# Performance work log

Measured on AMD Instinct MI355X. Metric: run time of the kernel, lower is better.

The kernel has to match this reference:

```python
import jax, jax.numpy as jnp
import numpy as np

VOCAB, EMB, HID, NCLS = 50000, 256, 512, 20
NCHARS, CEMB, CHID = 128, 64, 128
B, S, L = 128, 256, 16


def _gru(xw, h0, Wh, bh):
    """Run a GRU given precomputed input projections.
    xw: [N, T, 3H] = x @ Wi.T + bi (PyTorch gate order r,z,n)
    h0: [N, H]
    Returns (h_T [N,H], all_h [N,T,H])."""
    H = h0.shape[-1]
    def step(h, xw_t):
        gh = h @ Wh.T + bh  # [N, 3H]
        r = jax.nn.sigmoid(xw_t[:, :H] + gh[:, :H])
        z = jax.nn.sigmoid(xw_t[:, H:2 * H] + gh[:, H:2 * H])
        n = jnp.tanh(xw_t[:, 2 * H:] + r * gh[:, 2 * H:])
        h = (1.0 - z) * n + z * h
        return h, h
    hT, hs = jax.lax.scan(step, h0, jnp.swapaxes(xw, 0, 1))
    return hT, jnp.swapaxes(hs, 0, 1)


def setup_inputs() -> dict:
    key = jax.random.key(0)
    ks = jax.random.split(key, 16)
    sc = lambda *sh: 0.05
    inp = {}
    inp["x"] = jax.random.randint(ks[0], (B, S), 0, VOCAB)
    inp["x_chars"] = jax.random.randint(ks[1], (S, B, L), 0, NCHARS)
    inp["emb_w"] = jax.random.normal(ks[2], (VOCAB, EMB), jnp.float32) * 0.05
    inp["char_emb_w"] = jax.random.normal(ks[3], (NCHARS, CEMB), jnp.float32) * 0.05
    inp["char_Wi"] = jax.random.normal(ks[4], (3 * CHID, CEMB), jnp.float32) * 0.05
    inp["char_Wh"] = jax.random.normal(ks[5], (3 * CHID, CHID), jnp.float32) * 0.05
    inp["char_bi"] = jax.random.normal(ks[6], (3 * CHID,), jnp.float32) * 0.05
    inp["char_bh"] = jax.random.normal(ks[7], (3 * CHID,), jnp.float32) * 0.05
    D = EMB + CHID
    inp["gru_Wi"] = jax.random.normal(ks[8], (3 * HID, D), jnp.float32) * 0.05
    inp["gru_Wh"] = jax.random.normal(ks[9], (3 * HID, HID), jnp.float32) * 0.05
    inp["gru_bi"] = jax.random.normal(ks[10], (3 * HID,), jnp.float32) * 0.05
    inp["gru_bh"] = jax.random.normal(ks[11], (3 * HID,), jnp.float32) * 0.05
    inp["cls_W"] = jax.random.normal(ks[12], (NCLS, HID), jnp.float32) * 0.05
    inp["cls_b"] = jax.random.normal(ks[13], (NCLS,), jnp.float32) * 0.05
    return inp


def reference(x, x_chars, emb_w, char_emb_w, char_Wi, char_Wh, char_bi, char_bh,
              gru_Wi, gru_Wh, gru_bi, gru_bh, cls_W, cls_b):
    b, s = x.shape
    l = x_chars.shape[-1]
    # word embeddings [B,S,EMB]
    emb_x = emb_w[x]
    # char GRU: batch all S*B words at once (fuses the per-word Python loop)
    chid = char_Wh.shape[-1]
    flat = x_chars.reshape(s * b, l)           # [S*B, L]
    cemb = char_emb_w[flat]                    # [S*B, L, CEMB]
    cxw = jnp.einsum('ntd,gd->ntg', cemb, char_Wi) + char_bi
    h0c = jnp.zeros((s * b, chid), cemb.dtype)
    c_hT, _ = _gru(cxw, h0c, char_Wh, char_bh)  # [S*B, CHID]
    chars = jnp.swapaxes(c_hT.reshape(s, b, chid), 0, 1)  # [B,S,CHID]
    # word GRU over concat features
    feats = jnp.concatenate([emb_x, chars], axis=-1)       # [B,S,EMB+CHID]
    xw = jnp.einsum('btd,gd->btg', feats, gru_Wi) + gru_bi
    hid = gru_Wh.shape[-1]
    h0 = jnp.zeros((b, hid), feats.dtype)
    _, gru_out = _gru(xw, h0, gru_Wh, gru_bh)              # [B,S,HID]
    # dropout is identity in eval mode
    pred = jnp.einsum('bth,ch->btc', gru_out, cls_W) + cls_b
    return pred
```

## Files before the change

### kernel.cpp

```cpp
#include <hip/hip_runtime.h>
#include <cstdio>
#include <cstdint>

typedef __attribute__((ext_vector_type(8))) short short8;
typedef __attribute__((ext_vector_type(4))) float f32x4;

__device__ __forceinline__ f32x4 MFMA16(short8 a, short8 b, f32x4 c) {
  return __builtin_amdgcn_mfma_f32_16x16x32_bf16(a, b, c, 0, 0, 0);
}
__device__ __forceinline__ float bf2f(uint16_t u) {
  union { uint32_t u; float f; } v; v.u = ((uint32_t)u) << 16; return v.f;
}
__device__ __forceinline__ uint16_t f2bf(float f) {
  union { float f; uint32_t u; } v; v.f = f;
  uint32_t r = v.u + 0x7fffu + ((v.u >> 16) & 1u);
  return (uint16_t)(r >> 16);
}
__device__ __forceinline__ float fsig(float x) { return 1.0f / (1.0f + __expf(-x)); }
__device__ __forceinline__ float ftanh_(float x) { return 2.0f / (1.0f + __expf(-2.0f * x)) - 1.0f; }


#define OFF_CWI   0u
#define OFF_CWH   49152u
#define OFF_GWI   147456u
#define OFF_GWH   1327104u
#define OFF_CEMB  2899968u
#define OFF_CRZ   2916352u
#define OFF_CNI   2917376u
#define OFF_CNH   2917888u
#define OFF_WRZ   2918400u
#define OFF_WNI   2922496u
#define OFF_WNH   2924544u
#define OFF_CNT   2926592u
#define OFF_FEATS 3145728u
#define OFF_XW    28311552u
#define OFF_H     128974848u
#define WS_NEEDED 145752064ull

__global__ void k_prep(const float* __restrict__ cWi, const float* __restrict__ cWh,
                       const float* __restrict__ gWi, const float* __restrict__ gWh,
                       const float* __restrict__ cemb,
                       const float* __restrict__ cbi, const float* __restrict__ cbh,
                       const float* __restrict__ gbi, const float* __restrict__ gbh,
                       uint16_t* o_cWi, uint16_t* o_cWh, uint16_t* o_gWi, uint16_t* o_gWh,
                       uint16_t* o_cemb, float* o_crz, float* o_cni, float* o_cnh,
                       float* o_wrz, float* o_wni, float* o_wnh, unsigned* cnt)
{
  int g = blockIdx.x * 256 + threadIdx.x;
  int st = gridDim.x * 256;
  for (int i = g; i < 24576;  i += st) o_cWi[i] = f2bf(cWi[i]);
  for (int i = g; i < 49152;  i += st) o_cWh[i] = f2bf(cWh[i]);
  for (int i = g; i < 589824; i += st) o_gWi[i] = f2bf(gWi[i]);
  for (int i = g; i < 786432; i += st) o_gWh[i] = f2bf(gWh[i]);
  for (int i = g; i < 8192;   i += st) o_cemb[i] = f2bf(cemb[i]);
  for (int i = g; i < 256;  i += st) o_crz[i] = cbi[i] + cbh[i];
  for (int i = g; i < 128;  i += st) { o_cni[i] = cbi[256 + i]; o_cnh[i] = cbh[256 + i]; }
  for (int i = g; i < 1024; i += st) o_wrz[i] = gbi[i] + gbh[i];
  for (int i = g; i < 512;  i += st) { o_wni[i] = gbi[1024 + i]; o_wnh[i] = gbh[1024 + i]; }
  for (int i = g; i < 8192; i += st) cnt[i] = 0u;
}

__global__ void k_emb(const int* __restrict__ x, const float* __restrict__ embw,
                      uint16_t* __restrict__ feats)
{
  int n = blockIdx.x * 4 + (threadIdx.x >> 6);
  int lane = threadIdx.x & 63;
  int t = n >> 7, b = n & 127;
  int wid = x[b * 256 + t];
  float4 v = *(const float4*)(embw + (size_t)wid * 256 + lane * 4);
  uint16_t* dst = feats + (size_t)n * 384 + lane * 4;
  dst[0] = f2bf(v.x); dst[1] = f2bf(v.y); dst[2] = f2bf(v.z); dst[3] = f2bf(v.w);
}

__global__ __launch_bounds__(256, 1) void k_char(
    const int* __restrict__ xch, const uint16_t* __restrict__ cembw,
    const uint16_t* __restrict__ cWi, const uint16_t* __restrict__ cWh,
    const float* __restrict__ crz, const float* __restrict__ cni,
    const float* __restrict__ cnh, uint16_t* __restrict__ feats)
{
  extern __shared__ char lds[];
  uint16_t* WhL = (uint16_t*)lds;
  int*      idsL = (int*)(lds + 104448);
  uint16_t* hL  = (uint16_t*)(lds + 104448 + 4352);
  const int tid = threadIdx.x;
  const int wbase = blockIdx.x * 64;

  for (int i = tid; i < 384 * 16; i += 256) {
    int row = i >> 4, ch = i & 15;
    *(uint4*)(WhL + row * 136 + ch * 8) = *(const uint4*)(cWh + row * 128 + ch * 8);
  }
  for (int i = tid; i < 64 * 16; i += 256) {
    int w0 = i >> 4, p = i & 15;
    idsL[w0 * 17 + p] = xch[(wbase + w0) * 16 + p];
  }
  for (int i = tid; i < 64 * 136 / 2; i += 256) ((unsigned*)hL)[i] = 0u;
  __syncthreads();

  const int wv = tid >> 6, lane = tid & 63;
  const int q = lane >> 4, c = lane & 15;
  float br_[8], bz_[8], bni_[8], bnh_[8];
#pragma unroll
  for (int jb = 0; jb < 8; ++jb) {
    int j = jb * 16 + c;
    br_[jb] = crz[j]; bz_[jb] = crz[128 + j]; bni_[jb] = cni[j]; bnh_[jb] = cnh[j];
  }
  const int lwA = wv * 16 + c;
  const int lwD = wv * 16 + q * 4;

  for (int t = 0; t < 16; ++t) {
    f32x4 aRZ[16], aXN[8], aGN[8];
#pragma unroll
    for (int i = 0; i < 16; ++i) aRZ[i] = (f32x4)0.0f;
#pragma unroll
    for (int i = 0; i < 8; ++i) { aXN[i] = (f32x4)0.0f; aGN[i] = (f32x4)0.0f; }

    int id = idsL[lwA * 17 + t];
    const uint16_t* cerow = cembw + id * 64;
    short8 Ae0 = *(const short8*)(cerow + q * 8);
    short8 Ae1 = *(const short8*)(cerow + 32 + q * 8);
#pragma unroll
    for (int tl = 0; tl < 24; ++tl) {
      const uint16_t* wr = cWi + (tl * 16 + c) * 64 + q * 8;
      short8 B0 = *(const short8*)(wr);
      short8 B1 = *(const short8*)(wr + 32);
      if (tl < 16) { aRZ[tl] = MFMA16(Ae0, B0, aRZ[tl]); aRZ[tl] = MFMA16(Ae1, B1, aRZ[tl]); }
      else { aXN[tl - 16] = MFMA16(Ae0, B0, aXN[tl - 16]); aXN[tl - 16] = MFMA16(Ae1, B1, aXN[tl - 16]); }
    }
    short8 Ah[4];
#pragma unroll
    for (int kt = 0; kt < 4; ++kt) Ah[kt] = *(const short8*)(hL + lwA * 136 + kt * 32 + q * 8);
#pragma unroll
    for (int tl = 0; tl < 24; ++tl) {
#pragma unroll
      for (int kt = 0; kt < 4; ++kt) {
        short8 Bw = *(const short8*)(WhL + (tl * 16 + c) * 136 + kt * 32 + q * 8);
        if (tl < 16) aRZ[tl] = MFMA16(Ah[kt], Bw, aRZ[tl]);
        else aGN[tl - 16] = MFMA16(Ah[kt], Bw, aGN[tl - 16]);
      }
    }
#pragma unroll
    for (int jb = 0; jb < 8; ++jb) {
      int j = jb * 16 + c;
#pragma unroll
      for (int rg = 0; rg < 4; ++rg) {
        float r = fsig(aRZ[jb][rg] + br_[jb]);
        float z = fsig(aRZ[8 + jb][rg] + bz_[jb]);
        float n = ftanh_(aXN[jb][rg] + bni_[jb] + r * (aGN[jb][rg] + bnh_[jb]));
        int hoff = (lwD + rg) * 136 + j;
        float hold = bf2f(hL[hoff]);
        hL[hoff] = f2bf((1.0f - z) * n + z * hold);
      }
    }
  }
  __syncthreads();
  for (int i = tid; i < 64 * 128; i += 256) {
    int w0 = i >> 7, col = i & 127;
    feats[(size_t)(wbase + w0) * 384 + 256 + col] = hL[w0 * 136 + col];
  }
}

__global__ __launch_bounds__(256) void k_gemm_xw(
    const uint16_t* __restrict__ A, const uint16_t* __restrict__ Bm,
    uint16_t* __restrict__ C)
{
  __shared__ uint16_t AL[128 * 40];
  __shared__ uint16_t BL[128 * 40];
  const int tid = threadIdx.x;
  const int bm = blockIdx.x & 255, bn = blockIdx.x >> 8;
  const int m0 = bm * 128, n0 = bn * 128;
  const int wv = tid >> 6, lane = tid & 63, q = lane >> 4, c = lane & 15;
  const int vm = (wv >> 1) * 64, vn = (wv & 1) * 64;
  f32x4 acc[4][4];
#pragma unroll
  for (int mt = 0; mt < 4; ++mt)
#pragma unroll
    for (int nt = 0; nt < 4; ++nt) acc[mt][nt] = (f32x4)0.0f;

  for (int k0 = 0; k0 < 384; k0 += 32) {
    __syncthreads();
    for (int i2 = tid; i2 < 512; i2 += 256) {
      int row = i2 >> 2, cc = i2 & 3;
      *(uint4*)(AL + row * 40 + cc * 8) = *(const uint4*)(A + (size_t)(m0 + row) * 384 + k0 + cc * 8);
      *(uint4*)(BL + row * 40 + cc * 8) = *(const uint4*)(Bm + (size_t)(n0 + row) * 384 + k0 + cc * 8);
    }
    __syncthreads();
    short8 af[4], bfr[4];
#pragma unroll
    for (int mt = 0; mt < 4; ++mt) af[mt] = *(const short8*)(AL + (vm + mt * 16 + c) * 40 + q * 8);
#pragma unroll
    for (int nt = 0; nt < 4; ++nt) bfr[nt] = *(const short8*)(BL + (vn + nt * 16 + c) * 40 + q * 8);
#pragma unroll
    for (int mt = 0; mt < 4; ++mt)
#pragma unroll
      for (int nt = 0; nt < 4; ++nt) acc[mt][nt] = MFMA16(af[mt], bfr[nt], acc[mt][nt]);
  }
#pragma unroll
  for (int mt = 0; mt < 4; ++mt)
#pragma unroll
    for (int nt = 0; nt < 4; ++nt)
#pragma unroll
      for (int rg = 0; rg < 4; ++rg) {
        int m = m0 + vm + mt * 16 + q * 4 + rg;
        int n = n0 + vn + nt * 16 + c;
        C[(size_t)m * 1536 + n] = f2bf(acc[mt][nt][rg]);
      }
}

__global__ __launch_bounds__(64, 1) void k_gru(
    const uint16_t* __restrict__ xw, const uint16_t* __restrict__ gWh,
    const float* __restrict__ wrz, const float* __restrict__ wni,
    const float* __restrict__ wnh, uint16_t* __restrict__ H,
    unsigned* __restrict__ cnt)
{
  extern __shared__ char lds[];
  uint16_t* WhL = (uint16_t*)lds;
  const int tid = threadIdx.x;

  unsigned xcd;
  asm volatile("s_getreg_b32 %0, hwreg(HW_REG_XCC_ID, 0, 4)" : "=s"(xcd));
  unsigned* rdv = cnt + 4096;
  int myslot = 0;
  if (tid == 0) {
    myslot = (int)__hip_atomic_fetch_add(cnt + 4224 + xcd * 32, 1u, __ATOMIC_RELAXED, __HIP_MEMORY_SCOPE_AGENT);
    __hip_atomic_fetch_add(rdv, 1u, __ATOMIC_RELEASE, __HIP_MEMORY_SCOPE_AGENT);
  }
  myslot = __shfl(myslot, 0);
  {
    int sp = 0;
    while (__hip_atomic_load(rdv, __ATOMIC_ACQUIRE, __HIP_MEMORY_SCOPE_AGENT) < 128u) {
      __builtin_amdgcn_s_sleep(1);
      if (++sp > 10000000) break;
    }
  }
  unsigned G = 0, base = 0;
#pragma unroll
  for (int x2 = 0; x2 < 8; ++x2) {
    unsigned v = __hip_atomic_load(cnt + 4224 + x2 * 32, __ATOMIC_RELAXED, __HIP_MEMORY_SCOPE_AGENT) >> 4;
    if ((unsigned)x2 < xcd) base += v;
    G += v;
  }
  bool fastp; int gb, gc;
  if (G == 8u) { fastp = true; gb = (int)(base + ((unsigned)myslot >> 4)); gc = myslot & 15; }
  else         { fastp = false; gb = blockIdx.x & 7; gc = blockIdx.x >> 3; }

  const int m0 = gb * 16, j0 = gc * 32;
  unsigned* gflag  = cnt + ((gb * 16) << 5);
  unsigned* myflag = gflag + (gc << 5);
  unsigned* myCnt  = cnt + 4608 + (gb << 5);

  for (int i = tid; i < 96 * 64; i += 64) {
    int row = i >> 6, ch = i & 63;
    int gr = (row < 32) ? (j0 + row) : (row < 64) ? (512 + j0 + row - 32) : (1024 + j0 + row - 64);
    *(uint4*)(WhL + row * 520 + ch * 8) = *(const uint4*)(gWh + (size_t)gr * 512 + ch * 8);
  }
  const int q = tid >> 4, c = tid & 15;
  const int j1 = j0 + c, j2 = j0 + 16 + c;
  const float br0 = wrz[j1], br1 = wrz[j2];
  const float bz0 = wrz[512 + j1], bz1 = wrz[512 + j2];
  const float bi0 = wni[j1], bi1 = wni[j2];
  const float bh0 = wnh[j1], bh1 = wnh[j2];
  __syncthreads();

  uint16_t pf[4][6];
  {
    const uint16_t* xwt = xw + (size_t)m0 * 1536;
#pragma unroll
    for (int rg = 0; rg < 4; ++rg) {
      const uint16_t* rowp = xwt + (q * 4 + rg) * 1536;
      pf[rg][0] = rowp[j1];        pf[rg][1] = rowp[j2];
      pf[rg][2] = rowp[512 + j1];  pf[rg][3] = rowp[512 + j2];
      pf[rg][4] = rowp[1024 + j1]; pf[rg][5] = rowp[1024 + j2];
    }
  }
  float hold1[4] = {0.f, 0.f, 0.f, 0.f}, hold2[4] = {0.f, 0.f, 0.f, 0.f};

  for (int t = 0; t < 256; ++t) {
    f32x4 acc[6];
    float xn1[4], xn2[4];
#pragma unroll
    for (int rg = 0; rg < 4; ++rg) {
      acc[0][rg] = bf2f(pf[rg][0]); acc[1][rg] = bf2f(pf[rg][1]);
      acc[2][rg] = bf2f(pf[rg][2]); acc[3][rg] = bf2f(pf[rg][3]);
      acc[4][rg] = 0.0f; acc[5][rg] = 0.0f;
      xn1[rg] = bf2f(pf[rg][4]); xn2[rg] = bf2f(pf[rg][5]);
    }
    if (t > 0) {
      const uint16_t* hp = H + (size_t)((t - 1) * 128 + m0) * 512 + c * 512;
#pragma unroll 4
      for (int kt = 0; kt < 16; ++kt) {
        short8 a = *(const short8*)(hp + kt * 32 + q * 8);
#pragma unroll
        for (int tl = 0; tl < 6; ++tl) {
          short8 b = *(const short8*)(WhL + (tl * 16 + c) * 520 + kt * 32 + q * 8);
          acc[tl] = MFMA16(a, b, acc[tl]);
        }
      }
    }
    uint16_t* hcur = H + (size_t)(t * 128 + m0) * 512;
#pragma unroll
    for (int rg = 0; rg < 4; ++rg) {
      int m = q * 4 + rg;
      float r0 = fsig(acc[0][rg] + br0);
      float z0 = fsig(acc[2][rg] + bz0);
      float n0 = ftanh_(xn1[rg] + bi0 + r0 * (acc[4][rg] + bh0));
      float h0 = (1.0f - z0) * n0 + z0 * hold1[rg];
      hold1[rg] = h0;
      hcur[m * 512 + j1] = f2bf(h0);
      float r1 = fsig(acc[1][rg] + br1);
      float z1 = fsig(acc[3][rg] + bz1);
      float n1 = ftanh_(xn2[rg] + bi1 + r1 * (acc[5][rg] + bh1));
      float h1 = (1.0f - z1) * n1 + z1 * hold2[rg];
      hold2[rg] = h1;
      hcur[m * 512 + j2] = f2bf(h1);
    }
    if (t == 255) break;
    const unsigned tgt = (unsigned)(t + 1);
    if (fastp) {
      asm volatile("s_waitcnt vmcnt(0)" ::: "memory");
      if (tid == 0)
        __hip_atomic_store(myflag, tgt, __ATOMIC_RELAXED, __HIP_MEMORY_SCOPE_AGENT);
      {
        const uint16_t* xwn = xw + (size_t)((t + 1) * 128 + m0) * 1536;
#pragma unroll
        for (int rg = 0; rg < 4; ++rg) {
          const uint16_t* rowp = xwn + (q * 4 + rg) * 1536;
          pf[rg][0] = rowp[j1];        pf[rg][1] = rowp[j2];
          pf[rg][2] = rowp[512 + j1];  pf[rg][3] = rowp[512 + j2];
          pf[rg][4] = rowp[1024 + j1]; pf[rg][5] = rowp[1024 + j2];
        }
      }
      unsigned* watch = gflag + ((tid & 15) << 5);
      int sp = 0;
      for (;;) {
        unsigned v = __hip_atomic_load(watch, __ATOMIC_RELAXED, __HIP_MEMORY_SCOPE_AGENT);
        if (__all((int)(v >= tgt))) break;
        if (++sp > 2000000) break;
      }
      asm volatile("" ::: "memory");
    } else {
      {
        const uint16_t* xwn = xw + (size_t)((t + 1) * 128 + m0) * 1536;
#pragma unroll
        for (int rg = 0; rg < 4; ++rg) {
          const uint16_t* rowp = xwn + (q * 4 + rg) * 1536;
          pf[rg][0] = rowp[j1];        pf[rg][1] = rowp[j2];
          pf[rg][2] = rowp[512 + j1];  pf[rg][3] = rowp[512 + j2];
          pf[rg][4] = rowp[1024 + j1]; pf[rg][5] = rowp[1024 + j2];
        }
      }
      __threadfence();
      if (tid == 0) __hip_atomic_fetch_add(myCnt, 1u, __ATOMIC_RELAXED, __HIP_MEMORY_SCOPE_AGENT);
      const unsigned target = tgt * 16u;
      int sp = 0;
      while (__hip_atomic_load(myCnt, __ATOMIC_RELAXED, __HIP_MEMORY_SCOPE_AGENT) < target) {
        __builtin_amdgcn_s_sleep(1);
        if (++sp > 2000000) break;
      }
      __threadfence();
    }
  }
}

__global__ void k_cls(const uint16_t* __restrict__ H, const float* __restrict__ W,
                      const float* __restrict__ bb, float* __restrict__ out)
{
  int g = blockIdx.x * 256 + threadIdx.x;
  int c = g % 20, row = g / 20;
  int t = row >> 7, b = row & 127;
  const uint16_t* hp = H + (size_t)row * 512;
  const float* wp = W + c * 512;
  float acc = 0.0f;
  for (int i = 0; i < 512; i += 8) {
    uint4 hv = *(const uint4*)(hp + i);
    float4 w0 = *(const float4*)(wp + i);
    float4 w1 = *(const float4*)(wp + i + 4);
    acc += bf2f((uint16_t)hv.x) * w0.x + bf2f((uint16_t)(hv.x >> 16)) * w0.y
         + bf2f((uint16_t)hv.y) * w0.z + bf2f((uint16_t)(hv.y >> 16)) * w0.w
         + bf2f((uint16_t)hv.z) * w1.x + bf2f((uint16_t)(hv.z >> 16)) * w1.y
         + bf2f((uint16_t)hv.w) * w1.z + bf2f((uint16_t)(hv.w >> 16)) * w1.w;
  }
  out[((size_t)b * 256 + t) * 20 + c] = acc + bb[c];
}

extern "C" void kernel_launch(void* const* d_in, const int* in_sizes, int n_in,
                              void* d_out, int out_size, void* d_ws, size_t ws_size,
                              hipStream_t stream) {
  (void)in_sizes; (void)n_in; (void)out_size;
  const int*   x     = (const int*)d_in[0];
  const int*   xch   = (const int*)d_in[1];
  const float* embw  = (const float*)d_in[2];
  const float* cembw = (const float*)d_in[3];
  const float* cWi   = (const float*)d_in[4];
  const float* cWh   = (const float*)d_in[5];
  const float* cbi   = (const float*)d_in[6];
  const float* cbh   = (const float*)d_in[7];
  const float* gWi   = (const float*)d_in[8];
  const float* gWh   = (const float*)d_in[9];
  const float* gbi   = (const float*)d_in[10];
  const float* gbh   = (const float*)d_in[11];
  const float* clsW  = (const float*)d_in[12];
  const float* clsb  = (const float*)d_in[13];
  float* out = (float*)d_out;
  char* w = (char*)d_ws;

  if (ws_size < WS_NEEDED) { fprintf(stderr, "ws too small: %zu < %llu\n", ws_size, WS_NEEDED); return; }

  uint16_t* o_cWi  = (uint16_t*)(w + OFF_CWI);
  uint16_t* o_cWh  = (uint16_t*)(w + OFF_CWH);
  uint16_t* o_gWi  = (uint16_t*)(w + OFF_GWI);
  uint16_t* o_gWh  = (uint16_t*)(w + OFF_GWH);
  uint16_t* o_cemb = (uint16_t*)(w + OFF_CEMB);
  float* crz = (float*)(w + OFF_CRZ);
  float* cni = (float*)(w + OFF_CNI);
  float* cnh = (float*)(w + OFF_CNH);
  float* wrz = (float*)(w + OFF_WRZ);
  float* wni = (float*)(w + OFF_WNI);
  float* wnh = (float*)(w + OFF_WNH);
  unsigned* cnt = (unsigned*)(w + OFF_CNT);
  uint16_t* feats = (uint16_t*)(w + OFF_FEATS);
  uint16_t* xwb   = (uint16_t*)(w + OFF_XW);
  uint16_t* Hb    = (uint16_t*)(w + OFF_H);

  (void)hipFuncSetAttribute((const void*)k_char, hipFuncAttributeMaxDynamicSharedMemorySize, 126208);
  (void)hipFuncSetAttribute((const void*)k_gru,  hipFuncAttributeMaxDynamicSharedMemorySize, 99840);

  k_prep<<<512, 256, 0, stream>>>(cWi, cWh, gWi, gWh, cembw, cbi, cbh, gbi, gbh,
                                  o_cWi, o_cWh, o_gWi, o_gWh, o_cemb,
                                  crz, cni, cnh, wrz, wni, wnh, cnt);
  k_emb<<<8192, 256, 0, stream>>>(x, embw, feats);
  k_char<<<512, 256, 126208, stream>>>(xch, o_cemb, o_cWi, o_cWh, crz, cni, cnh, feats);
  k_gemm_xw<<<3072, 256, 0, stream>>>(feats, o_gWi, xwb);
  k_gru<<<128, 64, 99840, stream>>>(xwb, o_gWh, wrz, wni, wnh, Hb, cnt);
  k_cls<<<2560, 256, 0, stream>>>(Hb, clsW, clsb, out);
}
```

Before: 2.121 ms.

## Use leader-relayed step barrier in GRU, hoist loads, MFMA classifier

The recurrent GRU kernel now issues all hidden-state loads and the next-step input-projection prefetch before the MFMA loop, so memory latency overlaps compute. In the fast path only the first column block polls all sibling flags and then publishes a single go flag that the other blocks spin on, which reduces polling contention. The extra relay hop may add latency per step. The classifier is rewritten to use bf16 MFMA with weights converted in the prep kernel and staged in shared memory.

```diff
diff --git a/kernel.cpp b/kernel.cpp
--- a/kernel.cpp
+++ b/kernel.cpp
@@ -32,18 +32,20 @@
 #define OFF_WNI   2922496u
 #define OFF_WNH   2924544u
 #define OFF_CNT   2926592u
+#define OFF_CLSW  2990080u
 #define OFF_FEATS 3145728u
 #define OFF_XW    28311552u
 #define OFF_H     128974848u
-#define WS_NEEDED 145752064ull
+#define WS_NEEDED 162529280ull
 
 __global__ void k_prep(const float* __restrict__ cWi, const float* __restrict__ cWh,
                        const float* __restrict__ gWi, const float* __restrict__ gWh,
-                       const float* __restrict__ cemb,
+                       const float* __restrict__ cemb, const float* __restrict__ clsW,
                        const float* __restrict__ cbi, const float* __restrict__ cbh,
                        const float* __restrict__ gbi, const float* __restrict__ gbh,
                        uint16_t* o_cWi, uint16_t* o_cWh, uint16_t* o_gWi, uint16_t* o_gWh,
-                       uint16_t* o_cemb, float* o_crz, float* o_cni, float* o_cnh,
+                       uint16_t* o_cemb, uint16_t* o_clsW,
+                       float* o_crz, float* o_cni, float* o_cnh,
                        float* o_wrz, float* o_wni, float* o_wnh, unsigned* cnt)
 {
   int g = blockIdx.x * 256 + threadIdx.x;
@@ -53,6 +55,7 @@
   for (int i = g; i < 589824; i += st) o_gWi[i] = f2bf(gWi[i]);
   for (int i = g; i < 786432; i += st) o_gWh[i] = f2bf(gWh[i]);
   for (int i = g; i < 8192;   i += st) o_cemb[i] = f2bf(cemb[i]);
+  for (int i = g; i < 10240;  i += st) o_clsW[i] = f2bf(clsW[i]);
   for (int i = g; i < 256;  i += st) o_crz[i] = cbi[i] + cbh[i];
   for (int i = g; i < 128;  i += st) { o_cni[i] = cbi[256 + i]; o_cnh[i] = cbh[256 + i]; }
   for (int i = g; i < 1024; i += st) o_wrz[i] = gbi[i] + gbh[i];
@@ -244,9 +247,10 @@
   else         { fastp = false; gb = blockIdx.x & 7; gc = blockIdx.x >> 3; }
 
   const int m0 = gb * 16, j0 = gc * 32;
-  unsigned* gflag  = cnt + ((gb * 16) << 5);
-  unsigned* myflag = gflag + (gc << 5);
-  unsigned* myCnt  = cnt + 4608 + (gb << 5);
+  unsigned* arrbase = cnt + ((gb * 16) << 5);
+  unsigned* myflag  = arrbase + (gc << 5);
+  unsigned* goflag  = cnt + 5120 + (gb << 5);
+  unsigned* myCnt   = cnt + 4608 + (gb << 5);
 
   for (int i = tid; i < 96 * 64; i += 64) {
     int row = i >> 6, ch = i & 63;
@@ -275,6 +279,12 @@
   float hold1[4] = {0.f, 0.f, 0.f, 0.f}, hold2[4] = {0.f, 0.f, 0.f, 0.f};
 
   for (int t = 0; t < 256; ++t) {
+    short8 Ah[16];
+    if (t > 0) {
+      const uint16_t* hp = H + (size_t)((t - 1) * 128 + m0) * 512 + c * 512;
+#pragma unroll
+      for (int kt = 0; kt < 16; ++kt) Ah[kt] = *(const short8*)(hp + kt * 32 + q * 8);
+    }
     f32x4 acc[6];
     float xn1[4], xn2[4];
 #pragma unroll
@@ -284,15 +294,23 @@
       acc[4][rg] = 0.0f; acc[5][rg] = 0.0f;
       xn1[rg] = bf2f(pf[rg][4]); xn2[rg] = bf2f(pf[rg][5]);
     }
+    if (t < 255) {
+      const uint16_t* xwn = xw + (size_t)((t + 1) * 128 + m0) * 1536;
+#pragma unroll
+      for (int rg = 0; rg < 4; ++rg) {
+        const uint16_t* rowp = xwn + (q * 4 + rg) * 1536;
+        pf[rg][0] = rowp[j1];        pf[rg][1] = rowp[j2];
+        pf[rg][2] = rowp[512 + j1];  pf[rg][3] = rowp[512 + j2];
+        pf[rg][4] = rowp[1024 + j1]; pf[rg][5] = rowp[1024 + j2];
+      }
+    }
     if (t > 0) {
-      const uint16_t* hp = H + (size_t)((t - 1) * 128 + m0) * 512 + c * 512;
 #pragma unroll 4
       for (int kt = 0; kt < 16; ++kt) {
-        short8 a = *(const short8*)(hp + kt * 32 + q * 8);
 #pragma unroll
         for (int tl = 0; tl < 6; ++tl) {
           short8 b = *(const short8*)(WhL + (tl * 16 + c) * 520 + kt * 32 + q * 8);
-          acc[tl] = MFMA16(a, b, acc[tl]);
+          acc[tl] = MFMA16(Ah[kt], b, acc[tl]);
         }
       }
     }
@@ -319,35 +337,26 @@
       asm volatile("s_waitcnt vmcnt(0)" ::: "memory");
       if (tid == 0)
         __hip_atomic_store(myflag, tgt, __ATOMIC_RELAXED, __HIP_MEMORY_SCOPE_AGENT);
-      {
-        const uint16_t* xwn = xw + (size_t)((t + 1) * 128 + m0) * 1536;
-#pragma unroll
-        for (int rg = 0; rg < 4; ++rg) {
-          const uint16_t* rowp = xwn + (q * 4 + rg) * 1536;
-          pf[rg][0] = rowp[j1];        pf[rg][1] = rowp[j2];
-          pf[rg][2] = rowp[512 + j1];  pf[rg][3] = rowp[512 + j2];
-          pf[rg][4] = rowp[1024 + j1]; pf[rg][5] = rowp[1024 + j2];
+      if (gc == 0) {
+        unsigned* watch = arrbase + ((tid & 15) << 5);
+        int sp = 0;
+        for (;;) {
+          unsigned v = __hip_atomic_load(watch, __ATOMIC_RELAXED, __HIP_MEMORY_SCOPE_AGENT);
+          if (__all((int)(v >= tgt))) break;
+          if (++sp > 2000000) break;
         }
-      }
-      unsigned* watch = gflag + ((tid & 15) << 5);
-      int sp = 0;
-      for (;;) {
-        unsigned v = __hip_atomic_load(watch, __ATOMIC_RELAXED, __HIP_MEMORY_SCOPE_AGENT);
-        if (__all((int)(v >= tgt))) break;
-        if (++sp > 2000000) break;
+        if (tid == 0)
+          __hip_atomic_store(goflag, tgt, __ATOMIC_RELAXED, __HIP_MEMORY_SCOPE_AGENT);
+      } else {
+        int sp = 0;
+        for (;;) {
+          unsigned v = __hip_atomic_load(goflag, __ATOMIC_RELAXED, __HIP_MEMORY_SCOPE_AGENT);
+          if (v >= tgt) break;
+          if (++sp > 2000000) break;
+        }
       }
       asm volatile("" ::: "memory");
     } else {
-      {
-        const uint16_t* xwn = xw + (size_t)((t + 1) * 128 + m0) * 1536;
-#pragma unroll
-        for (int rg = 0; rg < 4; ++rg) {
-          const uint16_t* rowp = xwn + (q * 4 + rg) * 1536;
-          pf[rg][0] = rowp[j1];        pf[rg][1] = rowp[j2];
-          pf[rg][2] = rowp[512 + j1];  pf[rg][3] = rowp[512 + j2];
-          pf[rg][4] = rowp[1024 + j1]; pf[rg][5] = rowp[1024 + j2];
-        }
-      }
       __threadfence();
       if (tid == 0) __hip_atomic_fetch_add(myCnt, 1u, __ATOMIC_RELAXED, __HIP_MEMORY_SCOPE_AGENT);
       const unsigned target = tgt * 16u;
@@ -361,25 +370,40 @@
   }
 }
 
-__global__ void k_cls(const uint16_t* __restrict__ H, const float* __restrict__ W,
-                      const float* __restrict__ bb, float* __restrict__ out)
-{
-  int g = blockIdx.x * 256 + threadIdx.x;
-  int c = g % 20, row = g / 20;
-  int t = row >> 7, b = row & 127;
-  const uint16_t* hp = H + (size_t)row * 512;
-  const float* wp = W + c * 512;
-  float acc = 0.0f;
-  for (int i = 0; i < 512; i += 8) {
-    uint4 hv = *(const uint4*)(hp + i);
-    float4 w0 = *(const float4*)(wp + i);
-    float4 w1 = *(const float4*)(wp + i + 4);
-    acc += bf2f((uint16_t)hv.x) * w0.x + bf2f((uint16_t)(hv.x >> 16)) * w0.y
-         + bf2f((uint16_t)hv.y) * w0.z + bf2f((uint16_t)(hv.y >> 16)) * w0.w
-         + bf2f((uint16_t)hv.z) * w1.x + bf2f((uint16_t)(hv.z >> 16)) * w1.y
-         + bf2f((uint16_t)hv.w) * w1.z + bf2f((uint16_t)(hv.w >> 16)) * w1.w;
-  }
-  out[((size_t)b * 256 + t) * 20 + c] = acc + bb[c];
+__global__ __launch_bounds__(256) void k_cls(
+    const uint16_t* __restrict__ H, const uint16_t* __restrict__ Wb,
+    const float* __restrict__ bb, float* __restrict__ out)
+{
+  __shared__ uint16_t WsL[32 * 520];
+  const int tid = threadIdx.x;
+  for (int i = tid; i < 2048; i += 256) {
+    int row = i >> 6, col = (i & 63) * 8;
+    uint4 v = (row < 20) ? *(const uint4*)(Wb + row * 512 + col) : make_uint4(0u, 0u, 0u, 0u);
+    *(uint4*)(WsL + row * 520 + col) = v;
+  }
+  __syncthreads();
+  const int wv = tid >> 6, lane = tid & 63, q = lane >> 4, c = lane & 15;
+  const int rowbase = blockIdx.x * 64 + wv * 16;
+  f32x4 a0 = (f32x4)0.0f, a1 = (f32x4)0.0f;
+  const uint16_t* hp = H + (size_t)(rowbase + c) * 512 + q * 8;
+#pragma unroll
+  for (int kt = 0; kt < 16; ++kt) {
+    short8 a = *(const short8*)(hp + kt * 32);
+    short8 b0 = *(const short8*)(WsL + c * 520 + kt * 32 + q * 8);
+    short8 b1 = *(const short8*)(WsL + (16 + c) * 520 + kt * 32 + q * 8);
+    a0 = MFMA16(a, b0, a0);
+    a1 = MFMA16(a, b1, a1);
+  }
+  const float bias0 = bb[c];
+  const float bias1 = (c < 4) ? bb[16 + c] : 0.0f;
+#pragma unroll
+  for (int rg = 0; rg < 4; ++rg) {
+    int row = rowbase + q * 4 + rg;
+    int t = row >> 7, b = row & 127;
+    float* op = out + ((size_t)b * 256 + t) * 20;
+    op[c] = a0[rg] + bias0;
+    if (c < 4) op[16 + c] = a1[rg] + bias1;
+  }
 }
 
 extern "C" void kernel_launch(void* const* d_in, const int* in_sizes, int n_in,
@@ -410,6 +434,7 @@
   uint16_t* o_gWi  = (uint16_t*)(w + OFF_GWI);
   uint16_t* o_gWh  = (uint16_t*)(w + OFF_GWH);
   uint16_t* o_cemb = (uint16_t*)(w + OFF_CEMB);
+  uint16_t* o_clsW = (uint16_t*)(w + OFF_CLSW);
   float* crz = (float*)(w + OFF_CRZ);
   float* cni = (float*)(w + OFF_CNI);
   float* cnh = (float*)(w + OFF_CNH);
@@ -424,12 +449,12 @@
   (void)hipFuncSetAttribute((const void*)k_char, hipFuncAttributeMaxDynamicSharedMemorySize, 126208);
   (void)hipFuncSetAttribute((const void*)k_gru,  hipFuncAttributeMaxDynamicSharedMemorySize, 99840);
 
-  k_prep<<<512, 256, 0, stream>>>(cWi, cWh, gWi, gWh, cembw, cbi, cbh, gbi, gbh,
-                                  o_cWi, o_cWh, o_gWi, o_gWh, o_cemb,
+  k_prep<<<512, 256, 0, stream>>>(cWi, cWh, gWi, gWh, cembw, clsW, cbi, cbh, gbi, gbh,
+                                  o_cWi, o_cWh, o_gWi, o_gWh, o_cemb, o_clsW,
                                   crz, cni, cnh, wrz, wni, wnh, cnt);
   k_emb<<<8192, 256, 0, stream>>>(x, embw, feats);
   k_char<<<512, 256, 126208, stream>>>(xch, o_cemb, o_cWi, o_cWh, crz, cni, cnh, feats);
   k_gemm_xw<<<3072, 256, 0, stream>>>(feats, o_gWi, xwb);
   k_gru<<<128, 64, 99840, stream>>>(xwb, o_gWh, wrz, wni, wnh, Hb, cnt);
-  k_cls<<<2560, 256, 0, stream>>>(Hb, clsW, clsb, out);
-}
+  k_cls<<<512, 256, 0, stream>>>(Hb, o_clsW, clsb, out);
+}
```

Result: slower. 2.231 ms (+5.2%).
